# Optimization experiments

Measured on AMD Instinct MI355X. Metric: run time of the kernel, lower is better.

Reference implementation:

```python
import jax, jax.numpy as jnp
import numpy as np

# --- KAN_Convolution (b_spline) constants per init_kwargs ---
K = 3                      # kernel side
IN_F = K * K               # KANLinear in_features = prod(kernel_size)
GRID_SIZE = 5
SPLINE_ORDER = 3
GRID_LO, GRID_HI = -1.0, 1.0
STRIDE = (1, 1)
PAD = (1, 1)
DIL = (1, 1)


def make_grid():
    # efficient-kan grid: extended by spline_order knots on each side
    h = (GRID_HI - GRID_LO) / GRID_SIZE
    g = jnp.arange(-SPLINE_ORDER, GRID_SIZE + SPLINE_ORDER + 1, dtype=jnp.float32) * h + GRID_LO
    return jnp.broadcast_to(g, (IN_F, g.shape[0]))  # (in, G) with G = grid_size + 2*order + 1


def b_splines(x, grid):
    # x: (M, in) -> (M, in, grid_size + spline_order) via Cox-de-Boor recursion
    x = x[..., None]  # (M, in, 1)
    bases = ((x >= grid[:, :-1]) & (x < grid[:, 1:])).astype(x.dtype)
    for k in range(1, SPLINE_ORDER + 1):
        left = (x - grid[:, : -(k + 1)]) / (grid[:, k:-1] - grid[:, : -(k + 1)])
        right = (grid[:, k + 1 :] - x) / (grid[:, k + 1 :] - grid[:, 1:-k])
        bases = left * bases[..., :-1] + right * bases[..., 1:]
    return bases


def setup_inputs() -> dict:
    key = jax.random.key(0)
    k1, k2, k3, k4 = jax.random.split(key, 4)
    B, C, H, W = 8, 32, 64, 64
    x = jax.random.normal(k1, (B, C, H, W), jnp.float32)
    # KANLinear(in_features=9, out_features=1) parameters
    base_weight = jax.random.normal(k2, (1, IN_F), jnp.float32) * 0.3
    spline_weight = jax.random.normal(k3, (1, IN_F, GRID_SIZE + SPLINE_ORDER), jnp.float32) * 0.1
    spline_scaler = jax.random.normal(k4, (1, IN_F), jnp.float32) * 0.3 + 1.0
    return {
        "x": x,
        "base_weight": base_weight,
        "spline_weight": spline_weight,
        "spline_scaler": spline_scaler,
    }


def reference(x, base_weight, spline_weight, spline_scaler):
    B, C, H, W = x.shape
    # kan_conv2d: unfold each channel independently into (k*k)-patches,
    # then apply the shared KANLinear to every patch.
    patches = jax.lax.conv_general_dilated_patches(
        x.reshape(B * C, 1, H, W),
        filter_shape=(K, K),
        window_strides=STRIDE,
        padding=[(PAD[0], PAD[0]), (PAD[1], PAD[1])],
        rhs_dilation=DIL,
    )  # (B*C, K*K, Ho, Wo); feature order = row-major (kh, kw) like torch Unfold
    _, F, Ho, Wo = patches.shape
    p = jnp.transpose(patches, (0, 2, 3, 1)).reshape(-1, F)  # (M, 9)

    grid = make_grid()
    # base path: SiLU then linear (use_linear=True, base_activation=SiLU)
    base = jnp.dot(jax.nn.silu(p), base_weight.T)  # (M, 1)
    # spline path: B-spline bases contracted with scaled spline weights
    scaled_w = spline_weight * spline_scaler[..., None]  # (out, in, coef)
    sp = jnp.einsum("mic,oic->mo", b_splines(p, grid), scaled_w)  # (M, 1)

    out = (base + sp).reshape(B * C, Ho, Wo).reshape(B, C, Ho, Wo)
    return out
```

## Files before the change

kernel.cpp:

```cpp
#include <hip/hip_runtime.h>


constexpr int HW    = 64;
constexpr int PLANE = HW * HW;
constexpr int TILE  = 32;
constexpr int HT    = TILE + 2;
constexpr int HSTR  = 35;
constexpr int NC    = 31;

__global__ __launch_bounds__(256) void kan_conv(
    const float* __restrict__ x,
    const float* __restrict__ bw,
    const float* __restrict__ sw,
    const float* __restrict__ sc,
    float* __restrict__ out)
{
    __shared__ float  s_s[HT * HSTR];
    __shared__ float4 s_c[NC * 9];

    const int t = threadIdx.x;

    for (int p = t; p < NC * 9; p += 256) {
        const int m = p / 9, i = p - m * 9;
        const float vl = -6.2f + 0.4f * m;
        float y[4];
        #pragma unroll
        for (int j = 0; j < 4; ++j) {
            const float v = vl + (0.4f / 3.f) * j;
            y[j] = v / (1.f + __expf(-v));
        }
        const float bwi = bw[i];
        float4 c;
        c.x = y[0] * bwi;
        c.y = 0.5f * (-11.f * y[0] + 18.f * y[1] - 9.f * y[2] + 2.f * y[3]) * bwi;
        c.z = 4.5f * (2.f * y[0] - 5.f * y[1] + 4.f * y[2] - y[3]) * bwi;
        c.w = 4.5f * (-y[0] + 3.f * y[1] - 3.f * y[2] + y[3]) * bwi;
        const int ms = m - 10;
        if (ms >= 0 && ms <= 10) {
            const float sci = sc[i];
            float W[4];
            #pragma unroll
            for (int k = 0; k < 4; ++k) {
                const int q = ms + k;
                W[k] = (q >= 3 && q <= 10) ? sw[i * 8 + q - 3] * sci : 0.f;
            }
            c.x += (W[0] + 4.f * W[1] + W[2]) * (1.f / 6.f);
            c.y += (W[2] - W[0]) * 0.5f;
            c.z += (W[0] - 2.f * W[1] + W[2]) * 0.5f;
            c.w += (W[3] - W[0]) * (1.f / 6.f) + (W[1] - W[2]) * 0.5f;
        }
        s_c[m * 9 + i] = c;
    }

    const int bid   = blockIdx.x;
    const int plane = bid >> 2;
    const int th0   = ((bid >> 1) & 1) * TILE;
    const int tw0   = (bid & 1) * TILE;
    const float* __restrict__ xp = x + (size_t)plane * PLANE;

    for (int p = t; p < HT * HT; p += 256) {
        const int pr = p / HT, pc = p - pr * HT;
        const int gh = th0 - 1 + pr, gw = tw0 - 1 + pc;
        const bool valid = ((unsigned)gh < (unsigned)HW) && ((unsigned)gw < (unsigned)HW);
        const float v = valid ? xp[gh * HW + gw] : 0.f;
        float s = fmaf(v, 2.5f, 15.5f);
        s = fminf(fmaxf(s, 0.f), 30.99f);
        s_s[pr * HSTR + pc] = s;
    }
    __syncthreads();

    const int tx = t & 7, ty = t >> 3;
    const float* __restrict__ fb = &s_s[ty * HSTR + tx * 4];
    float acc0 = 0.f, acc1 = 0.f, acc2 = 0.f, acc3 = 0.f;

    #pragma unroll
    for (int r = 0; r < 3; ++r) {
        float u[6];
        const char* cp[6];
        #pragma unroll
        for (int j = 0; j < 6; ++j) {
            const float s  = fb[r * HSTR + j];
            const float fm = floorf(s);
            u[j] = s - fm;
            cp[j] = (const char*)s_c + (unsigned)(fm * 144.f);
        }
        #pragma unroll
        for (int j = 0; j < 6; ++j) {
            const int kmin = (j >= 2) ? (j - 2) : 0;
            const int kmax = (j <= 3) ? j : 3;
            #pragma unroll
            for (int k = kmin; k <= kmax; ++k) {
                const int i = r * 3 + (j - k);
                const float4 c = *(const float4*)(cp[j] + i * 16);
                const float s1 = fmaf(fmaf(fmaf(c.w, u[j], c.z), u[j], c.y), u[j], c.x);
                if      (k == 0) acc0 += s1;
                else if (k == 1) acc1 += s1;
                else if (k == 2) acc2 += s1;
                else             acc3 += s1;
            }
        }
    }

    float4 o4 = {acc0, acc1, acc2, acc3};
    *(float4*)&out[(size_t)plane * PLANE + (th0 + ty) * HW + tw0 + tx * 4] = o4;
}

extern "C" void kernel_launch(void* const* d_in, const int* in_sizes, int n_in,
                              void* d_out, int out_size, void* d_ws, size_t ws_size,
                              hipStream_t stream) {
    const float* x  = (const float*)d_in[0];
    const float* bw = (const float*)d_in[1];
    const float* sw = (const float*)d_in[2];
    const float* sc = (const float*)d_in[3];
    float* o = (float*)d_out;

    kan_conv<<<1024, 256, 0, stream>>>(x, bw, sw, sc, o);
}
```

Baseline: 66.52 us.

## Shrink tiles to 16x32, hoist global loads, precompute spline index/fraction in LDS

Halves the tile height so each thread computes 2 outputs instead of 4, doubling the grid to 2048 blocks for more parallelism. The global loads are issued before the per-block coefficient-table setup so their latency overlaps that work. The floor and fraction are computed once per halo pixel and stored as a float2 in shared memory, instead of being recomputed by every thread that reads the pixel. In exchange there is more halo overhead per output, more redundant coefficient-table setup across blocks, larger LDS use per block, and a launch-bounds occupancy hint.

```diff
diff --git a/kernel.cpp b/kernel.cpp
--- a/kernel.cpp
+++ b/kernel.cpp
@@ -3,22 +3,44 @@
 
 constexpr int HW    = 64;
 constexpr int PLANE = HW * HW;
-constexpr int TILE  = 32;
-constexpr int HT    = TILE + 2;
-constexpr int HSTR  = 35;
+constexpr int TH    = 16;
+constexpr int TW    = 32;
+constexpr int HR    = TH + 2;
+constexpr int HC    = TW + 2;
+constexpr int NPIX  = HR * HC;
+constexpr int SF    = 37;
 constexpr int NC    = 31;
 
-__global__ __launch_bounds__(256) void kan_conv(
+__global__ __launch_bounds__(256, 5) void kan_conv(
     const float* __restrict__ x,
     const float* __restrict__ bw,
     const float* __restrict__ sw,
     const float* __restrict__ sc,
     float* __restrict__ out)
 {
-    __shared__ float  s_s[HT * HSTR];
+    __shared__ float2 s_f[HR * SF];
     __shared__ float4 s_c[NC * 9];
 
-    const int t = threadIdx.x;
+    const int t   = threadIdx.x;
+    const int bid = blockIdx.x;
+    const int plane = bid >> 3;
+    const int th0   = ((bid >> 1) & 3) * TH;
+    const int tw0   = (bid & 1) * TW;
+    const float* __restrict__ xp = x + (size_t)plane * PLANE;
+
+    const int p0 = t, p1 = t + 256, p2 = t + 512;
+    const int pr0 = p0 / HC, pc0 = p0 - pr0 * HC;
+    const int pr1 = p1 / HC, pc1 = p1 - pr1 * HC;
+    const int pr2 = p2 / HC, pc2 = p2 - pr2 * HC;
+    const int gh0 = th0 - 1 + pr0, gw0 = tw0 - 1 + pc0;
+    const int gh1 = th0 - 1 + pr1, gw1 = tw0 - 1 + pc1;
+    const int gh2 = th0 - 1 + pr2, gw2 = tw0 - 1 + pc2;
+    const bool ok0 = ((unsigned)gh0 < (unsigned)HW) && ((unsigned)gw0 < (unsigned)HW);
+    const bool ok1 = ((unsigned)gh1 < (unsigned)HW) && ((unsigned)gw1 < (unsigned)HW);
+    const bool ok2 = (p2 < NPIX) && ((unsigned)gh2 < (unsigned)HW) && ((unsigned)gw2 < (unsigned)HW);
+    const float v0 = ok0 ? xp[gh0 * HW + gw0] : 0.f;
+    const float v1 = ok1 ? xp[gh1 * HW + gw1] : 0.f;
+    const float v2 = ok2 ? xp[gh2 * HW + gw2] : 0.f;
 
     for (int p = t; p < NC * 9; p += 256) {
         const int m = p / 9, i = p - m * 9;
@@ -52,57 +74,57 @@
         s_c[m * 9 + i] = c;
     }
 
-    const int bid   = blockIdx.x;
-    const int plane = bid >> 2;
-    const int th0   = ((bid >> 1) & 1) * TILE;
-    const int tw0   = (bid & 1) * TILE;
-    const float* __restrict__ xp = x + (size_t)plane * PLANE;
-
-    for (int p = t; p < HT * HT; p += 256) {
-        const int pr = p / HT, pc = p - pr * HT;
-        const int gh = th0 - 1 + pr, gw = tw0 - 1 + pc;
-        const bool valid = ((unsigned)gh < (unsigned)HW) && ((unsigned)gw < (unsigned)HW);
-        const float v = valid ? xp[gh * HW + gw] : 0.f;
-        float s = fmaf(v, 2.5f, 15.5f);
+    {
+        float s = fmaf(v0, 2.5f, 15.5f);
         s = fminf(fmaxf(s, 0.f), 30.99f);
-        s_s[pr * HSTR + pc] = s;
+        const float fm = floorf(s);
+        s_f[pr0 * SF + pc0] = make_float2(s - fm, __uint_as_float((unsigned)(fm * 144.f)));
+    }
+    {
+        float s = fmaf(v1, 2.5f, 15.5f);
+        s = fminf(fmaxf(s, 0.f), 30.99f);
+        const float fm = floorf(s);
+        s_f[pr1 * SF + pc1] = make_float2(s - fm, __uint_as_float((unsigned)(fm * 144.f)));
+    }
+    if (p2 < NPIX) {
+        float s = fmaf(v2, 2.5f, 15.5f);
+        s = fminf(fmaxf(s, 0.f), 30.99f);
+        const float fm = floorf(s);
+        s_f[pr2 * SF + pc2] = make_float2(s - fm, __uint_as_float((unsigned)(fm * 144.f)));
     }
     __syncthreads();
 
-    const int tx = t & 7, ty = t >> 3;
-    const float* __restrict__ fb = &s_s[ty * HSTR + tx * 4];
-    float acc0 = 0.f, acc1 = 0.f, acc2 = 0.f, acc3 = 0.f;
+    const int tx = t & 15, ty = t >> 4;
+    const float2* __restrict__ fb = &s_f[ty * SF + 2 * tx];
+    float acc0 = 0.f, acc1 = 0.f;
 
     #pragma unroll
     for (int r = 0; r < 3; ++r) {
-        float u[6];
-        const char* cp[6];
+        float u[4];
+        const char* cp[4];
         #pragma unroll
-        for (int j = 0; j < 6; ++j) {
-            const float s  = fb[r * HSTR + j];
-            const float fm = floorf(s);
-            u[j] = s - fm;
-            cp[j] = (const char*)s_c + (unsigned)(fm * 144.f);
+        for (int j = 0; j < 4; ++j) {
+            const float2 d = fb[r * SF + j];
+            u[j] = d.x;
+            cp[j] = (const char*)s_c + __float_as_uint(d.y);
         }
         #pragma unroll
-        for (int j = 0; j < 6; ++j) {
+        for (int j = 0; j < 4; ++j) {
             const int kmin = (j >= 2) ? (j - 2) : 0;
-            const int kmax = (j <= 3) ? j : 3;
+            const int kmax = (j <= 1) ? j : 1;
             #pragma unroll
             for (int k = kmin; k <= kmax; ++k) {
                 const int i = r * 3 + (j - k);
                 const float4 c = *(const float4*)(cp[j] + i * 16);
                 const float s1 = fmaf(fmaf(fmaf(c.w, u[j], c.z), u[j], c.y), u[j], c.x);
-                if      (k == 0) acc0 += s1;
-                else if (k == 1) acc1 += s1;
-                else if (k == 2) acc2 += s1;
-                else             acc3 += s1;
+                if (k == 0) acc0 += s1;
+                else        acc1 += s1;
             }
         }
     }
 
-    float4 o4 = {acc0, acc1, acc2, acc3};
-    *(float4*)&out[(size_t)plane * PLANE + (th0 + ty) * HW + tw0 + tx * 4] = o4;
+    float2 o2 = {acc0, acc1};
+    *(float2*)&out[(size_t)plane * PLANE + (th0 + ty) * HW + tw0 + 2 * tx] = o2;
 }
 
 extern "C" void kernel_launch(void* const* d_in, const int* in_sizes, int n_in,
@@ -114,5 +136,5 @@
     const float* sc = (const float*)d_in[3];
     float* o = (float*)d_out;
 
-    kan_conv<<<1024, 256, 0, stream>>>(x, bw, sw, sc, o);
+    kan_conv<<<2048, 256, 0, stream>>>(x, bw, sw, sc, o);
 }
```

Measured after the change: 65.57 us. About the same (-1.4%).
